# Kernel tuning notes

Hardware: AMD Instinct MI355X
Metric: run time of the kernel (lower is better)

The kernel has to match this reference:

```python
import jax, jax.numpy as jnp
import numpy as np

C = 256
LN_EPS = 1e-5

def setup_inputs() -> dict:
    key = jax.random.key(0)
    ks = jax.random.split(key, 12)
    B, M, N = 8, 4096, 4096
    scale = 1.0 / np.sqrt(C)
    inp = {
        'x': jax.random.normal(ks[0], (B, M, C), jnp.float32),
        'y': jax.random.normal(ks[1], (B, N, C), jnp.float32),
        'Wq': jax.random.normal(ks[2], (C, C), jnp.float32) * scale,
        'bq': jnp.zeros((C,), jnp.float32),
        'Wk': jax.random.normal(ks[3], (C, C), jnp.float32) * scale,
        'bk': jnp.zeros((C,), jnp.float32),
        'Wv': jax.random.normal(ks[4], (C, C), jnp.float32) * scale,
        'bv': jnp.zeros((C,), jnp.float32),
        'Wo': jax.random.normal(ks[5], (C, C), jnp.float32) * (scale * 1e-5),
        'bo': jnp.zeros((C,), jnp.float32),
        'gamma': jnp.ones((C,), jnp.float32),
        'beta': jnp.zeros((C,), jnp.float32),
    }
    return inp

def reference(x, y, Wq, bq, Wk, bk, Wv, bv, Wo, bo, gamma, beta):
    # projections (torch Linear: x @ W.T + b)
    q = x @ Wq.T + bq                      # [B,M,C]
    k = y @ Wk.T + bk                      # [B,N,C]
    v = y @ Wv.T + bv                      # [B,N,C]
    # scaled dot-product attention with explicit score matrix
    w = jnp.einsum('bmc,bnc->bmn', q, k) * (C ** -0.5)  # [B,M,N]
    w = jax.nn.softmax(w, axis=-1)
    h = jnp.einsum('bmn,bnc->bmc', w, v)   # [B,M,C]
    h = h @ Wo.T + bo
    z = x + h
    # LayerNorm over last dim
    mu = jnp.mean(z, axis=-1, keepdims=True)
    var = jnp.var(z, axis=-1, keepdims=True)
    out = (z - mu) * jax.lax.rsqrt(var + LN_EPS) * gamma + beta
    return out
```

## Files before the change

### kernel.cpp

```cpp
#include <hip/hip_runtime.h>
#include <hip/hip_bf16.h>

#define C_DIM 256
#define QSCALE 0.09016844f
#define WO_SCALE 1048576.0f
#define WO_INV   9.5367431640625e-07f

typedef __attribute__((ext_vector_type(8))) short bf16x8;
typedef __attribute__((ext_vector_type(4))) float f32x4;
typedef __attribute__((ext_vector_type(16))) float f32x16;

__device__ __forceinline__ void gload16(const unsigned char* g, unsigned char* l) {
    __builtin_amdgcn_global_load_lds(
        (const __attribute__((address_space(1))) void*)g,
        (__attribute__((address_space(3))) void*)l, 16, 0, 0);
}

__global__ void cvt_w_kernel(const float* __restrict__ w0, const float* __restrict__ w1,
                             const float* __restrict__ w2, const float* __restrict__ w3,
                             unsigned char* __restrict__ o0, unsigned char* __restrict__ o1,
                             unsigned char* __restrict__ o2, unsigned char* __restrict__ o3) {
    int i = (blockIdx.x * 256 + threadIdx.x) * 4;
    #pragma unroll
    for (int wsel = 0; wsel < 4; ++wsel) {
        const float* w = wsel == 0 ? w0 : (wsel == 1 ? w1 : (wsel == 2 ? w2 : w3));
        unsigned char* o = wsel == 0 ? o0 : (wsel == 1 ? o1 : (wsel == 2 ? o2 : o3));
        const float sc = (wsel == 3) ? WO_SCALE : 1.0f;
        float4 v = *reinterpret_cast<const float4*>(w + i);
        unsigned p = __builtin_amdgcn_cvt_pk_fp8_f32(v.x * sc, v.y * sc, 0, false);
        p = __builtin_amdgcn_cvt_pk_fp8_f32(v.z * sc, v.w * sc, p, true);
        *reinterpret_cast<unsigned*>(o + i) = p;
    }
}

__global__ __launch_bounds__(256, 1)
void proj_kernel(const float* __restrict__ x, const float* __restrict__ y,
                 const unsigned char* __restrict__ wq8, const unsigned char* __restrict__ wk8,
                 const unsigned char* __restrict__ wv8,
                 const float* __restrict__ bqp, const float* __restrict__ bkp,
                 const float* __restrict__ bvp,
                 unsigned char* __restrict__ qo, unsigned char* __restrict__ ko,
                 unsigned char* __restrict__ vo)
{
    __shared__ __align__(16) unsigned char ldsW[65536];
    __shared__ __align__(16) unsigned char ldsA[32768];

    const int which = blockIdx.x >> 8;
    const int tile = blockIdx.x & 255;
    const float* in = (which == 0) ? x : y;
    const unsigned char* wsrc = (which == 0) ? wq8 : (which == 1 ? wk8 : wv8);
    const float* bias = (which == 0) ? bqp : (which == 1 ? bkp : bvp);
    unsigned char* out = (which == 0) ? qo : (which == 1 ? ko : vo);
    const float oscale = (which == 0) ? QSCALE : 1.0f;

    const int tid = threadIdx.x;
    const int rowbase = tile * 128;

    #pragma unroll
    for (int it = 0; it < 16; ++it) {
        int G = it * 256 + tid;
        int c = G >> 4, p = G & 15;
        gload16(wsrc + c * 256 + ((p ^ (c & 15)) << 4), ldsW + G * 16);
    }
    #pragma unroll
    for (int it = 0; it < 32; ++it) {
        int e = it * 1024 + tid * 4;
        int r = e >> 8, c4 = e & 255;
        float4 v = *reinterpret_cast<const float4*>(in + (size_t)(rowbase + r) * C_DIM + c4);
        unsigned p = __builtin_amdgcn_cvt_pk_fp8_f32(v.x, v.y, 0, false);
        p = __builtin_amdgcn_cvt_pk_fp8_f32(v.z, v.w, p, true);
        int g = (c4 >> 4) ^ (r & 15);
        *reinterpret_cast<unsigned*>(ldsA + r * 256 + g * 16 + (c4 & 12)) = p;
    }
    __syncthreads();

    const int lane = tid & 63, wave = tid >> 6;
    const int lrow = lane & 15, lkq = lane >> 4;
    const int koff = (lkq & 1) << 3;
    const int kg = lkq >> 1;

    #pragma unroll
    for (int ms = 0; ms < 2; ++ms) {
        const int arow = wave * 32 + ms * 16 + lrow;
        long a[8];
        #pragma unroll
        for (int ks = 0; ks < 8; ++ks)
            a[ks] = *reinterpret_cast<const long*>(
                ldsA + arow * 256 + (((ks * 2 + kg) ^ (arow & 15)) << 4) + koff);

        f32x4 acc[16];
        #pragma unroll
        for (int nf = 0; nf < 16; ++nf) acc[nf] = f32x4{0.f, 0.f, 0.f, 0.f};

        #pragma unroll
        for (int nf = 0; nf < 16; ++nf) {
            const int c = nf * 16 + lrow;
            const unsigned char* wb = ldsW + c * 256;
            const int cx = c & 15;
            #pragma unroll
            for (int ks = 0; ks < 8; ++ks) {
                long b = *reinterpret_cast<const long*>(wb + (((ks * 2 + kg) ^ cx) << 4) + koff);
                acc[nf] = __builtin_amdgcn_mfma_f32_16x16x32_fp8_fp8(a[ks], b, acc[nf], 0, 0, 0);
            }
        }

        const int base = rowbase + wave * 32 + ms * 16 + lkq * 4;
        if (which != 2) {
            const int rsw = (which == 1) ? (base & 8) : 0;
            #pragma unroll
            for (int nf = 0; nf < 16; ++nf) {
                float bv = bias[nf * 16 + lrow];
                float v0 = (acc[nf][0] + bv) * oscale, v1 = (acc[nf][1] + bv) * oscale;
                float v2 = (acc[nf][2] + bv) * oscale, v3 = (acc[nf][3] + bv) * oscale;
                unsigned p = __builtin_amdgcn_cvt_pk_fp8_f32(v0, v1, 0, false);
                p = __builtin_amdgcn_cvt_pk_fp8_f32(v2, v3, p, true);
                int col = (nf * 16 + lrow) ^ rsw;
                unsigned char* o = out + (size_t)base * C_DIM + col;
                o[0]   = (unsigned char)p;
                o[256] = (unsigned char)(p >> 8);
                o[512] = (unsigned char)(p >> 16);
                o[768] = (unsigned char)(p >> 24);
            }
        } else {
            int bb = base >> 12, n0 = base & 4095;
            #pragma unroll
            for (int nf = 0; nf < 16; ++nf) {
                float bv = bias[nf * 16 + lrow];
                float v0 = acc[nf][0] + bv, v1 = acc[nf][1] + bv;
                float v2 = acc[nf][2] + bv, v3 = acc[nf][3] + bv;
                unsigned p = __builtin_amdgcn_cvt_pk_fp8_f32(v0, v1, 0, false);
                p = __builtin_amdgcn_cvt_pk_fp8_f32(v2, v3, p, true);
                int c = nf * 16 + lrow;
                *reinterpret_cast<unsigned*>(vo + ((size_t)bb * C_DIM + c) * 4096 + (n0 ^ (c & 8))) = p;
            }
        }
    }
}

__global__ __launch_bounds__(512, 1)
void attn_kernel(const unsigned char* __restrict__ qg, const unsigned char* __restrict__ kg,
                 const unsigned char* __restrict__ vtg, unsigned short* __restrict__ hg)
{
    __shared__ __align__(16) unsigned char smb[98304];

    const int tid = threadIdx.x;
    const int lane = tid & 63;
    const int w = tid >> 6;
    const int wq = w & 3;
    const int half = w >> 2;
    const int l31 = lane & 31;
    const int hi5 = lane >> 5;
    const int ksw = l31 & 15;
    const int hsw = ((l31 >> 3) & 1) << 3;
    const int vsw = ((l31 >> 2) & 1);

    const int batch = blockIdx.x & 7;
    const int mt = blockIdx.x >> 3;
    const size_t q0 = (size_t)batch * 4096 + mt * 128 + wq * 32;

    const unsigned char* kbase = kg + ((size_t)batch * 4096 + half * 2048) * 256;
    const unsigned char* vbase = vtg + (size_t)batch * 256 * 4096 + half * 2048;

    long qf[16];
    #pragma unroll
    for (int ks = 0; ks < 16; ++ks)
        qf[ks] = *reinterpret_cast<const long*>(qg + (q0 + l31) * 256 + ks * 16 + hi5 * 8);

    f32x16 o[8];
    #pragma unroll
    for (int cb = 0; cb < 8; ++cb) {
        #pragma unroll
        for (int r = 0; r < 16; ++r) o[cb][r] = 0.f;
    }

    float m_run = -__builtin_inff();
    float lsum = 0.f;

    auto stage = [&](int kb, int vb, int kt) {
        const int kv0 = kt * 32;
        unsigned char* lk = smb + (half * 2 + kb) * 8192;
        unsigned char* lv = smb + 32768 + (half * 3 + vb) * 8192;
        #pragma unroll
        for (int i = 0; i < 2; ++i) {
            int g = wq * 128 + i * 64 + lane;
            int row = g >> 4, pos = g & 15;
            gload16(kbase + (size_t)(kv0 + row) * 256 + ((pos ^ (row & 15)) << 4), lk + g * 16);
        }
        #pragma unroll
        for (int i = 0; i < 2; ++i) {
            int s = wq * 128 + i * 64 + lane;
            int c = s >> 1;
            int k2 = (s & 1) ^ ((s >> 3) & 1);
            gload16(vbase + (size_t)c * 4096 + kv0 + k2 * 16, lv + s * 16);
        }
    };

    auto do_S = [&](int kb, f32x16& sreg) {
        const unsigned char* krow = smb + (half * 2 + kb) * 8192 + l31 * 256 + ((hi5 * 8) ^ hsw);
        #pragma unroll
        for (int r = 0; r < 16; ++r) sreg[r] = 0.f;
        __builtin_amdgcn_s_setprio(1);
        #pragma unroll
        for (int ks = 0; ks < 16; ++ks) {
            long a0 = *reinterpret_cast<const long*>(krow + ((ks ^ ksw) << 4));
            sreg = __builtin_amdgcn_mfma_f32_32x32x16_fp8_fp8(a0, qf[ks], sreg, 0, 0, 0);
        }
        __builtin_amdgcn_s_setprio(0);
    };

    auto do_SMPV = [&](f32x16& sreg, int vb) {
        float mloc = sreg[0];
        #pragma unroll
        for (int r = 1; r < 16; ++r) mloc = fmaxf(mloc, sreg[r]);
        mloc = fmaxf(mloc, __shfl_xor(mloc, 32, 64));

        if (__any(mloc > m_run + 8.0f)) {
            float mn = fmaxf(m_run, mloc);
            float al = exp2f(m_run - mn);
            m_run = mn;
            lsum *= al;
            #pragma unroll
            for (int cb = 0; cb < 8; ++cb) {
                #pragma unroll
                for (int r = 0; r < 16; ++r) o[cb][r] *= al;
            }
        }

        float ts = 0.f;
        #pragma unroll
        for (int r = 0; r < 16; ++r) { sreg[r] = exp2f(sreg[r] - m_run); ts += sreg[r]; }
        ts += __shfl_xor(ts, 32, 64);
        lsum += ts;

        unsigned Wu[8];
        #pragma unroll
        for (int a = 0; a < 8; ++a) {
            unsigned p = __builtin_amdgcn_cvt_pk_fp8_f32(sreg[4 * a], sreg[4 * a + 1], 0, false);
            Wu[a] = __builtin_amdgcn_cvt_pk_fp8_f32(sreg[4 * a + 2], sreg[4 * a + 3], p, true);
        }

        const bool h = (hi5 != 0);
        const unsigned char* vrow = smb + 32768 + (half * 3 + vb) * 8192
                                    + l31 * 32 + ((hi5 * 8) ^ hsw);
        __builtin_amdgcn_s_setprio(1);
        #pragma unroll
        for (int ksv = 0; ksv < 2; ++ksv) {
            unsigned snd = h ? Wu[2 * ksv] : Wu[2 * ksv + 1];
            unsigned rcv = __shfl_xor(snd, 32, 64);
            unsigned wlo = h ? rcv : Wu[2 * ksv];
            unsigned whi = h ? Wu[2 * ksv + 1] : rcv;
            long pb = (long)(((unsigned long long)whi << 32) | (unsigned long long)wlo);
            const int k2s = (ksv ^ vsw) << 4;
            #pragma unroll
            for (int cb = 0; cb < 8; ++cb) {
                long vf = *reinterpret_cast<const long*>(vrow + cb * 1024 + k2s);
                o[cb] = __builtin_amdgcn_mfma_f32_32x32x16_fp8_fp8(vf, pb, o[cb], 0, 0, 0);
            }
        }
        __builtin_amdgcn_s_setprio(0);
    };

    stage(0, 0, 0);
    __syncthreads();

    f32x16 s0;
    if (half == 0) {
        int vcur = 0, vnxt = 1;
        for (int kt = 0; kt < 64; ++kt) {
            if (kt < 63) stage((kt + 1) & 1, vnxt, kt + 1);
            do_S(kt & 1, s0);
            do_SMPV(s0, vcur);
            __syncthreads();
            vcur = vnxt; vnxt = (vnxt == 2) ? 0 : vnxt + 1;
        }
    } else {
        int vprv = 2, vcur = 0, vnxt = 1;
        for (int kt = 0; kt < 64; ++kt) {
            if (kt < 63) stage((kt + 1) & 1, vnxt, kt + 1);
            if (kt > 0) do_SMPV(s0, vprv);
            do_S(kt & 1, s0);
            __syncthreads();
            vprv = vcur; vcur = vnxt; vnxt = (vnxt == 2) ? 0 : vnxt + 1;
        }
        do_SMPV(s0, vprv);
    }

    __syncthreads();

    unsigned short* pub = (unsigned short*)smb;
    float* ml = (float*)(smb + 90112);

    if (half == 1) {
        if (hi5 == 0) {
            ml[(wq * 32 + l31) * 2]     = m_run;
            ml[(wq * 32 + l31) * 2 + 1] = lsum;
        }
        unsigned short* prow = pub + (wq * 32 + l31) * 256;
        const int cxor = (l31 & 15) << 2;
        #pragma unroll
        for (int cb = 0; cb < 8; ++cb) {
            #pragma unroll
            for (int rp = 0; rp < 8; ++rp) {
                const int r = 2 * rp;
                unsigned wpk;
                float lo = o[cb][r], hi_ = o[cb][r + 1];
                asm("v_cvt_pk_bf16_f32 %0, %1, %2" : "=v"(wpk) : "v"(lo), "v"(hi_));
                int c = cb * 32 + (r & 3) + 8 * (r >> 2) + 4 * hi5;
                *reinterpret_cast<unsigned*>(prow + (c ^ cxor)) = wpk;
            }
        }
    }
    __syncthreads();

    if (half == 0) {
        float m1 = ml[(wq * 32 + l31) * 2];
        float l1 = ml[(wq * 32 + l31) * 2 + 1];
        float mm = fmaxf(m_run, m1);
        float a0 = exp2f(m_run - mm), a1 = exp2f(m1 - mm);
        float lt = lsum * a0 + l1 * a1;
        float rinv = 1.0f / lt;
        float f0 = a0 * rinv, f1 = a1 * rinv;

        const unsigned short* prow = pub + (wq * 32 + l31) * 256;
        const int cxor = (l31 & 15) << 2;
        unsigned short* tr = (unsigned short*)(smb + 65536 + wq * 4608);
        #pragma unroll
        for (int cc = 0; cc < 4; ++cc) {
            #pragma unroll
            for (int cbh = 0; cbh < 2; ++cbh) {
                const int cb = cc * 2 + cbh;
                #pragma unroll
                for (int rp = 0; rp < 8; ++rp) {
                    const int r = 2 * rp;
                    int c = cb * 32 + (r & 3) + 8 * (r >> 2) + 4 * hi5;
                    unsigned pk = *reinterpret_cast<const unsigned*>(prow + (c ^ cxor));
                    union { unsigned u; float f; } b0, b1;
                    b0.u = pk << 16; b1.u = pk & 0xffff0000u;
                    float v_lo = o[cb][r]     * f0 + b0.f * f1;
                    float v_hi = o[cb][r + 1] * f0 + b1.f * f1;
                    unsigned wpk;
                    asm("v_cvt_pk_bf16_f32 %0, %1, %2" : "=v"(wpk) : "v"(v_lo), "v"(v_hi));
                    int c_local = 32 * cbh + (r & 3) + 8 * (r >> 2) + 4 * hi5;
                    *reinterpret_cast<unsigned*>(tr + l31 * 72 + c_local) = wpk;
                }
            }
            __builtin_amdgcn_s_waitcnt(0);
            #pragma unroll
            for (int i = 0; i < 4; ++i) {
                int idx = i * 64 + lane;
                int q = idx >> 3, ch = idx & 7;
                uint4 d = *reinterpret_cast<const uint4*>(tr + q * 72 + ch * 8);
                *reinterpret_cast<uint4*>(hg + (q0 + q) * 256 + cc * 64 + ch * 8) = d;
            }
        }
    }
}

__global__ __launch_bounds__(256, 1)
void out_kernel(const unsigned short* __restrict__ hb, const unsigned char* __restrict__ wo8,
                const float* __restrict__ bo, const float* __restrict__ xg,
                const float* __restrict__ gamma, const float* __restrict__ beta,
                float* __restrict__ outg)
{
    __shared__ __align__(16) unsigned char ldsW[65536];
    __shared__ __align__(16) unsigned char ldsA[32768];

    const int tid = threadIdx.x;
    const int rowbase = blockIdx.x * 128;

    #pragma unroll
    for (int it = 0; it < 16; ++it) {
        int G = it * 256 + tid;
        int c = G >> 4, p = G & 15;
        gload16(wo8 + c * 256 + ((p ^ (c & 15)) << 4), ldsW + G * 16);
    }
    #pragma unroll
    for (int it = 0; it < 16; ++it) {
        int e = it * 2048 + tid * 8;
        int r = e >> 8, c8 = e & 255;
        uint4 d = *reinterpret_cast<const uint4*>(hb + (size_t)(rowbase + r) * C_DIM + c8);
        union { unsigned u; float f; } f0, f1, f2, f3, f4, f5, f6, f7;
        f0.u = d.x << 16; f1.u = d.x & 0xffff0000u;
        f2.u = d.y << 16; f3.u = d.y & 0xffff0000u;
        f4.u = d.z << 16; f5.u = d.z & 0xffff0000u;
        f6.u = d.w << 16; f7.u = d.w & 0xffff0000u;
        unsigned p0 = __builtin_amdgcn_cvt_pk_fp8_f32(f0.f, f1.f, 0, false);
        p0 = __builtin_amdgcn_cvt_pk_fp8_f32(f2.f, f3.f, p0, true);
        unsigned p1 = __builtin_amdgcn_cvt_pk_fp8_f32(f4.f, f5.f, 0, false);
        p1 = __builtin_amdgcn_cvt_pk_fp8_f32(f6.f, f7.f, p1, true);
        int g = (c8 >> 4) ^ (r & 15);
        uint2 pk; pk.x = p0; pk.y = p1;
        *reinterpret_cast<uint2*>(ldsA + r * 256 + g * 16 + (c8 & 8)) = pk;
    }
    __syncthreads();

    const int lane = tid & 63, wave = tid >> 6;
    const int lrow = lane & 15, lkq = lane >> 4;
    const int koff = (lkq & 1) << 3;
    const int kg = lkq >> 1;

    #pragma unroll
    for (int ms = 0; ms < 2; ++ms) {
        const int arow = wave * 32 + ms * 16 + lrow;
        long a[8];
        #pragma unroll
        for (int ks = 0; ks < 8; ++ks)
            a[ks] = *reinterpret_cast<const long*>(
                ldsA + arow * 256 + (((ks * 2 + kg) ^ (arow & 15)) << 4) + koff);

        f32x4 acc[16];
        #pragma unroll
        for (int nf = 0; nf < 16; ++nf) acc[nf] = f32x4{0.f, 0.f, 0.f, 0.f};

        #pragma unroll
        for (int nf = 0; nf < 16; ++nf) {
            const int c = nf * 16 + lrow;
            const unsigned char* wb = ldsW + c * 256;
            const int cx = c & 15;
            #pragma unroll
            for (int ks = 0; ks < 8; ++ks) {
                long b = *reinterpret_cast<const long*>(wb + (((ks * 2 + kg) ^ cx) << 4) + koff);
                acc[nf] = __builtin_amdgcn_mfma_f32_16x16x32_fp8_fp8(a[ks], b, acc[nf], 0, 0, 0);
            }
        }

        const int base = rowbase + wave * 32 + ms * 16 + lkq * 4;

        #pragma unroll
        for (int nf = 0; nf < 16; ++nf) {
            float bv = bo[nf * 16 + lrow];
            #pragma unroll
            for (int r = 0; r < 4; ++r) {
                size_t row = base + r;
                acc[nf][r] = acc[nf][r] * WO_INV + bv + xg[row * C_DIM + nf * 16 + lrow];
            }
        }

        float mu[4], rstd[4];
        #pragma unroll
        for (int r = 0; r < 4; ++r) {
            float s1 = 0.f, s2 = 0.f;
            #pragma unroll
            for (int nf = 0; nf < 16; ++nf) { float v = acc[nf][r]; s1 += v; s2 += v * v; }
            #pragma unroll
            for (int off = 1; off < 16; off <<= 1) {
                s1 += __shfl_xor(s1, off, 64);
                s2 += __shfl_xor(s2, off, 64);
            }
            float m = s1 * (1.f / 256.f);
            mu[r] = m;
            rstd[r] = rsqrtf(s2 * (1.f / 256.f) - m * m + 1e-5f);
        }

        #pragma unroll
        for (int nf = 0; nf < 16; ++nf) {
            float g = gamma[nf * 16 + lrow];
            float bt = beta[nf * 16 + lrow];
            #pragma unroll
            for (int r = 0; r < 4; ++r) {
                size_t row = base + r;
                outg[row * C_DIM + nf * 16 + lrow] = (acc[nf][r] - mu[r]) * rstd[r] * g + bt;
            }
        }
    }
}

extern "C" void kernel_launch(void* const* d_in, const int* in_sizes, int n_in,
                              void* d_out, int out_size, void* d_ws, size_t ws_size,
                              hipStream_t stream) {
    const float* x     = (const float*)d_in[0];
    const float* y     = (const float*)d_in[1];
    const float* Wq    = (const float*)d_in[2];
    const float* bq    = (const float*)d_in[3];
    const float* Wk    = (const float*)d_in[4];
    const float* bk    = (const float*)d_in[5];
    const float* Wv    = (const float*)d_in[6];
    const float* bv    = (const float*)d_in[7];
    const float* Wo    = (const float*)d_in[8];
    const float* bo    = (const float*)d_in[9];
    const float* gamma = (const float*)d_in[10];
    const float* beta  = (const float*)d_in[11];
    float* out = (float*)d_out;

    unsigned char* ws = (unsigned char*)d_ws;
    unsigned char* wq8 = ws;
    unsigned char* wk8 = ws + 65536;
    unsigned char* wv8 = ws + 131072;
    unsigned char* wo8 = ws + 196608;
    unsigned char* q_b = ws + 262144;
    unsigned char* k_b = q_b + 8388608;
    unsigned char* v_b = k_b + 8388608;
    unsigned short* h_b = (unsigned short*)(v_b + 8388608);

    cvt_w_kernel<<<64, 256, 0, stream>>>(Wq, Wk, Wv, Wo, wq8, wk8, wv8, wo8);

    proj_kernel<<<768, 256, 0, stream>>>(x, y, wq8, wk8, wv8, bq, bk, bv, q_b, k_b, v_b);

    attn_kernel<<<256, 512, 0, stream>>>(q_b, k_b, v_b, h_b);

    out_kernel<<<256, 256, 0, stream>>>(h_b, wo8, bo, x, gamma, beta, out);
}
```

Before: 196.3 us.

## Software-pipeline QK and PV MFMAs by interleaving previous tile's PV with current S

The attention loop is restructured so every wave computes S for tile kt while running the P·V MFMAs of tile kt-1 inside the same unrolled loop. The softmax step now only produces packed fp8 P operands, which are carried into the next iteration. This replaces the earlier scheme where the two wave halves were offset to overlap softmax with MFMA across waves. It aims to keep the matrix pipe busy during softmax and exp latency, at the cost of more live registers and a one-tile lag in the V buffer rotation.

Result: faster. 187.3 us (-4.6%).

```diff
diff --git a/kernel.cpp b/kernel.cpp
--- a/kernel.cpp
+++ b/kernel.cpp
@@ -208,7 +208,43 @@
         __builtin_amdgcn_s_setprio(0);
     };
 
-    auto do_SMPV = [&](f32x16& sreg, int vb) {
+    auto do_S_PV = [&](int kb, f32x16& sreg, long pb0, long pb1, int vb) {
+        const unsigned char* krow = smb + (half * 2 + kb) * 8192 + l31 * 256 + ((hi5 * 8) ^ hsw);
+        const unsigned char* vrow = smb + 32768 + (half * 3 + vb) * 8192
+                                    + l31 * 32 + ((hi5 * 8) ^ hsw);
+        #pragma unroll
+        for (int r = 0; r < 16; ++r) sreg[r] = 0.f;
+        __builtin_amdgcn_s_setprio(1);
+        #pragma unroll
+        for (int i = 0; i < 16; ++i) {
+            long a0 = *reinterpret_cast<const long*>(krow + ((i ^ ksw) << 4));
+            sreg = __builtin_amdgcn_mfma_f32_32x32x16_fp8_fp8(a0, qf[i], sreg, 0, 0, 0);
+            const int ksv = i >> 3, cb = i & 7;
+            long vf = *reinterpret_cast<const long*>(vrow + cb * 1024 + (((ksv ^ vsw)) << 4));
+            o[cb] = __builtin_amdgcn_mfma_f32_32x32x16_fp8_fp8(
+                vf, ksv ? pb1 : pb0, o[cb], 0, 0, 0);
+        }
+        __builtin_amdgcn_s_setprio(0);
+    };
+
+    auto do_PV = [&](long pb0, long pb1, int vb) {
+        const unsigned char* vrow = smb + 32768 + (half * 3 + vb) * 8192
+                                    + l31 * 32 + ((hi5 * 8) ^ hsw);
+        __builtin_amdgcn_s_setprio(1);
+        #pragma unroll
+        for (int ksv = 0; ksv < 2; ++ksv) {
+            const int k2s = (ksv ^ vsw) << 4;
+            #pragma unroll
+            for (int cb = 0; cb < 8; ++cb) {
+                long vf = *reinterpret_cast<const long*>(vrow + cb * 1024 + k2s);
+                o[cb] = __builtin_amdgcn_mfma_f32_32x32x16_fp8_fp8(
+                    vf, ksv ? pb1 : pb0, o[cb], 0, 0, 0);
+            }
+        }
+        __builtin_amdgcn_s_setprio(0);
+    };
+
+    auto do_SM = [&](f32x16& sreg, long& pb0, long& pb1) {
         float mloc = sreg[0];
         #pragma unroll
         for (int r = 1; r < 16; ++r) mloc = fmaxf(mloc, sreg[r]);
@@ -232,17 +268,14 @@
         ts += __shfl_xor(ts, 32, 64);
         lsum += ts;
 
-        unsigned Wu[8];
-        #pragma unroll
-        for (int a = 0; a < 8; ++a) {
+        unsigned Wu[4];
+        #pragma unroll
+        for (int a = 0; a < 4; ++a) {
             unsigned p = __builtin_amdgcn_cvt_pk_fp8_f32(sreg[4 * a], sreg[4 * a + 1], 0, false);
             Wu[a] = __builtin_amdgcn_cvt_pk_fp8_f32(sreg[4 * a + 2], sreg[4 * a + 3], p, true);
         }
 
         const bool h = (hi5 != 0);
-        const unsigned char* vrow = smb + 32768 + (half * 3 + vb) * 8192
-                                    + l31 * 32 + ((hi5 * 8) ^ hsw);
-        __builtin_amdgcn_s_setprio(1);
         #pragma unroll
         for (int ksv = 0; ksv < 2; ++ksv) {
             unsigned snd = h ? Wu[2 * ksv] : Wu[2 * ksv + 1];
@@ -250,40 +283,30 @@
             unsigned wlo = h ? rcv : Wu[2 * ksv];
             unsigned whi = h ? Wu[2 * ksv + 1] : rcv;
             long pb = (long)(((unsigned long long)whi << 32) | (unsigned long long)wlo);
-            const int k2s = (ksv ^ vsw) << 4;
-            #pragma unroll
-            for (int cb = 0; cb < 8; ++cb) {
-                long vf = *reinterpret_cast<const long*>(vrow + cb * 1024 + k2s);
-                o[cb] = __builtin_amdgcn_mfma_f32_32x32x16_fp8_fp8(vf, pb, o[cb], 0, 0, 0);
-            }
-        }
-        __builtin_amdgcn_s_setprio(0);
+            if (ksv == 0) pb0 = pb; else pb1 = pb;
+        }
     };
 
     stage(0, 0, 0);
     __syncthreads();
 
     f32x16 s0;
-    if (half == 0) {
-        int vcur = 0, vnxt = 1;
-        for (int kt = 0; kt < 64; ++kt) {
-            if (kt < 63) stage((kt + 1) & 1, vnxt, kt + 1);
-            do_S(kt & 1, s0);
-            do_SMPV(s0, vcur);
-            __syncthreads();
-            vcur = vnxt; vnxt = (vnxt == 2) ? 0 : vnxt + 1;
-        }
-    } else {
-        int vprv = 2, vcur = 0, vnxt = 1;
-        for (int kt = 0; kt < 64; ++kt) {
-            if (kt < 63) stage((kt + 1) & 1, vnxt, kt + 1);
-            if (kt > 0) do_SMPV(s0, vprv);
-            do_S(kt & 1, s0);
-            __syncthreads();
-            vprv = vcur; vcur = vnxt; vnxt = (vnxt == 2) ? 0 : vnxt + 1;
-        }
-        do_SMPV(s0, vprv);
-    }
+    long pb0 = 0, pb1 = 0;
+
+    stage(1, 1, 1);
+    do_S(0, s0);
+    do_SM(s0, pb0, pb1);
+    __syncthreads();
+
+    int vprv = 0, vcur = 1, vnxt = 2;
+    for (int kt = 1; kt < 64; ++kt) {
+        if (kt < 63) stage((kt + 1) & 1, vnxt, kt + 1);
+        do_S_PV(kt & 1, s0, pb0, pb1, vprv);
+        do_SM(s0, pb0, pb1);
+        __syncthreads();
+        vprv = vcur; vcur = vnxt; vnxt = (vnxt == 2) ? 0 : vnxt + 1;
+    }
+    do_PV(pb0, pb1, vprv);
 
     __syncthreads();
 
```
